# Kernel optimization log

Measured on AMD Instinct MI355X. Metric: run time of the kernel, lower is better.

## Reference

```python
import jax, jax.numpy as jnp
import numpy as np

N = 500000
C = 128
G = 4096


def setup_inputs() -> dict:
    key = jax.random.key(0)
    ks = jax.random.split(key, 6)
    x = jax.random.normal(ks[0], (N, C), dtype=jnp.float32)
    proj_w = jax.random.normal(ks[1], (C, C), dtype=jnp.float32) * (1.0 / np.sqrt(C))
    proj_b = jax.random.normal(ks[2], (C,), dtype=jnp.float32) * 0.01
    score_w = jax.random.normal(ks[3], (1, C), dtype=jnp.float32) * (1.0 / np.sqrt(C))
    score_b = jax.random.normal(ks[4], (1,), dtype=jnp.float32) * 0.01
    batch = jnp.sort(jax.random.randint(ks[5], (N,), 0, G, dtype=jnp.int32))
    return {"x": x, "proj_w": proj_w, "proj_b": proj_b,
            "score_w": score_w, "score_b": score_b,
            "batch": batch, "num_graphs": G}


def reference(x, proj_w, proj_b, score_w, score_b, batch, num_graphs):
    # h = tanh(Linear(x)); s = Linear(h) -> [N]
    h = jnp.tanh(x @ proj_w.T + proj_b)
    s = (h @ score_w.T + score_b)[:, 0]  # [N]
    # segment softmax over nodes of each graph
    m = jax.ops.segment_max(s, batch, num_segments=num_graphs)  # [G]
    m = jnp.where(jnp.isfinite(m), m, 0.0)  # guard empty segments
    e = jnp.exp(s - m[batch])
    denom = jax.ops.segment_sum(e, batch, num_segments=num_graphs)  # [G]
    w = e / jnp.maximum(denom[batch], 1e-30)  # [N]
    # weighted scatter-sum of raw features
    pooled = jax.ops.segment_sum(x * w[:, None], batch, num_segments=num_graphs)  # [G, C]
    return pooled
```

## Files before the change

### kernel.cpp

```cpp
#include <hip/hip_runtime.h>
#include <hip/hip_bf16.h>
#include <float.h>
#include <math.h>

#define CDIM 128

typedef __attribute__((ext_vector_type(8))) short short8v;
typedef __attribute__((ext_vector_type(4))) short short4v;
typedef __attribute__((ext_vector_type(4))) float f32x4;

__device__ __forceinline__ short bf16b(float f) {
    __hip_bfloat16 h = __float2bfloat16(f);
    return __builtin_bit_cast(short, h);
}

__device__ __forceinline__ float tanh_fast(float y) {
    float e = __expf(2.0f * y);
    return 1.0f - 2.0f / (e + 1.0f);
}

__device__ __forceinline__ int lower_bound_i(const int* __restrict__ b, int n, int v) {
    int lo = 0, hi = n;
    while (lo < hi) { int mid = (lo + hi) >> 1; if (b[mid] < v) lo = mid + 1; else hi = mid; }
    return lo;
}

__global__ void seg_bounds_kernel(const int* __restrict__ batch, int N, int G,
                                  int* __restrict__ seg) {
    int g = blockIdx.x * blockDim.x + threadIdx.x;
    if (g < G) seg[g] = lower_bound_i(batch, N, g);
    if (g == 0) seg[G] = N;
}

__global__ void wconv_kernel(const float* __restrict__ proj_w, short* __restrict__ wfrag) {
    int tid = blockIdx.x * 256 + threadIdx.x;
    int f = tid >> 6, l = tid & 63;
    int c  = ((f >> 2) << 4) | (l & 15);
    int k0 = ((f & 3) << 5) | ((l >> 4) << 3);
    short8v v;
    #pragma unroll
    for (int j = 0; j < 8; ++j) v[j] = bf16b(proj_w[c * CDIM + k0 + j]);
    ((short8v*)wfrag)[tid] = v;
}

__launch_bounds__(256, 4)
__global__ void pool_kernel(const float* __restrict__ x,
                            const short* __restrict__ wfrag,
                            const float* __restrict__ proj_b,
                            const float* __restrict__ score_w,
                            const float* __restrict__ score_b,
                            const int* __restrict__ seg,
                            float* __restrict__ out,
                            int N) {
    __shared__ __align__(16) short XsB[64 * 128];
    __shared__ float ps[64 * 4];

    const int g = blockIdx.x;
    const int t = threadIdx.x;
    const int lane = t & 63;
    const int w = t >> 6;
    const int start = seg[g];
    const int cnt = seg[g + 1] - start;
    float4* og4 = (float4*)(out + (size_t)g * CDIM);

    if (cnt <= 0) {
        if (t < 32) og4[t] = make_float4(0.f, 0.f, 0.f, 0.f);
        return;
    }

    short8v wf[2][4];
    {
        const short8v* wfg = (const short8v*)wfrag;
        #pragma unroll
        for (int j = 0; j < 2; ++j)
            #pragma unroll
            for (int ks = 0; ks < 4; ++ks)
                wf[j][ks] = wfg[((((w << 1) | j) << 2 | ks) << 6) | lane];
    }
    const int al = lane & 15, ah = lane >> 4;
    float swl[2], pbl[2];
    #pragma unroll
    for (int j = 0; j < 2; ++j) {
        swl[j] = score_w[(((w << 1) | j) << 4) + al];
        pbl[j] = proj_b[(((w << 1) | j) << 4) + al];
    }
    const float sb = score_b[0];

    const float4* __restrict__ x4 = (const float4*)x;
    const int g8 = t >> 5;
    const int c4 = t & 31;

    float m_run = -FLT_MAX, l_run = 0.0f;
    float4 pa = make_float4(0.f, 0.f, 0.f, 0.f);

    for (int cb = 0; cb < cnt; cb += 64) {
        const int rem = cnt - cb;

        float4 xr[8];
        #pragma unroll
        for (int i = 0; i < 8; ++i) {
            int row = g8 + (i << 3);
            size_t gr = (size_t)min(start + cb + row, N - 1);
            xr[i] = x4[gr * 32 + c4];
        }
        #pragma unroll
        for (int i = 0; i < 8; ++i) {
            int row = g8 + (i << 3);
            short4v b;
            b[0] = bf16b(xr[i].x); b[1] = bf16b(xr[i].y);
            b[2] = bf16b(xr[i].z); b[3] = bf16b(xr[i].w);
            *(short4v*)&XsB[(row << 7) | ((c4 << 2) ^ ((row & 7) << 3))] = b;
        }
        __syncthreads();

        #pragma unroll
        for (int rt = 0; rt < 4; ++rt) {
            const int arow = (rt << 4) | al;
            const int rsw = (arow & 7) << 3;
            f32x4 a0 = (f32x4){0.f, 0.f, 0.f, 0.f};
            f32x4 a1 = (f32x4){0.f, 0.f, 0.f, 0.f};
            #pragma unroll
            for (int ks = 0; ks < 4; ++ks) {
                short8v af = *(const short8v*)&XsB[(arow << 7) | (((ks << 5) | (ah << 3)) ^ rsw)];
                a0 = __builtin_amdgcn_mfma_f32_16x16x32_bf16(af, wf[0][ks], a0, 0, 0, 0);
                a1 = __builtin_amdgcn_mfma_f32_16x16x32_bf16(af, wf[1][ks], a1, 0, 0, 0);
            }
            #pragma unroll
            for (int r = 0; r < 4; ++r) {
                float s = swl[0] * tanh_fast(a0[r] + pbl[0])
                        + swl[1] * tanh_fast(a1[r] + pbl[1]);
                s += __shfl_xor(s, 1); s += __shfl_xor(s, 2);
                s += __shfl_xor(s, 4); s += __shfl_xor(s, 8);
                if (al == 0) ps[(((rt << 4) | (ah << 2) | r) << 2) | w] = s;
            }
        }
        __syncthreads();

        float4 pp = *(const float4*)&ps[lane << 2];
        float sv = (lane < rem) ? (pp.x + pp.y + pp.z + pp.w + sb) : -FLT_MAX;
        float mx = sv;
        #pragma unroll
        for (int m = 1; m < 64; m <<= 1) mx = fmaxf(mx, __shfl_xor(mx, m));
        const float m_new = fmaxf(m_run, mx);
        float ev = (lane < rem) ? __expf(sv - m_new) : 0.f;
        float ssum = ev;
        #pragma unroll
        for (int m = 1; m < 64; m <<= 1) ssum += __shfl_xor(ssum, m);
        const float sc = __expf(m_run - m_new);
        m_run = m_new;
        l_run = l_run * sc + ssum;
        pa.x *= sc; pa.y *= sc; pa.z *= sc; pa.w *= sc;

        #pragma unroll
        for (int i = 0; i < 8; ++i) {
            float em = __shfl(ev, g8 + (i << 3));
            pa.x += em * xr[i].x; pa.y += em * xr[i].y;
            pa.z += em * xr[i].z; pa.w += em * xr[i].w;
        }
    }

    float* red = (float*)XsB;
    *(float4*)&red[(g8 << 7) + (c4 << 2)] = pa;
    __syncthreads();
    if (t < 32) {
        float4 v = make_float4(0.f, 0.f, 0.f, 0.f);
        #pragma unroll
        for (int j = 0; j < 8; ++j) {
            float4 r = *(const float4*)&red[(j << 7) + (t << 2)];
            v.x += r.x; v.y += r.y; v.z += r.z; v.w += r.w;
        }
        const float inv = 1.0f / fmaxf(l_run, 1e-30f);
        v.x *= inv; v.y *= inv; v.z *= inv; v.w *= inv;
        og4[t] = v;
    }
}

extern "C" void kernel_launch(void* const* d_in, const int* in_sizes, int n_in,
                              void* d_out, int out_size, void* d_ws, size_t ws_size,
                              hipStream_t stream) {
    const float* x       = (const float*)d_in[0];
    const float* proj_w  = (const float*)d_in[1];
    const float* proj_b  = (const float*)d_in[2];
    const float* score_w = (const float*)d_in[3];
    const float* score_b = (const float*)d_in[4];
    const int*   batch   = (const int*)d_in[5];

    const int N = in_sizes[0] / CDIM;
    const int G = out_size / CDIM;

    int*   seg   = (int*)d_ws;
    short* wfrag = (short*)((char*)d_ws + (((size_t)(G + 1) * 4 + 255) & ~(size_t)255));

    seg_bounds_kernel<<<(G + 255) / 256, 256, 0, stream>>>(batch, N, G, seg);
    wconv_kernel<<<8, 256, 0, stream>>>(proj_w, wfrag);
    pool_kernel<<<G, 256, 0, stream>>>(x, wfrag, proj_b, score_w, score_b,
                                       seg, (float*)d_out, N);
}
```

Before: 100.5 us.

## Double-buffer x chunks in LDS via async global_load_lds prefetch

After: 104.5 us. +4.0%, slower.

```diff
diff --git a/kernel.cpp b/kernel.cpp
--- a/kernel.cpp
+++ b/kernel.cpp
@@ -6,7 +6,6 @@
 #define CDIM 128
 
 typedef __attribute__((ext_vector_type(8))) short short8v;
-typedef __attribute__((ext_vector_type(4))) short short4v;
 typedef __attribute__((ext_vector_type(4))) float f32x4;
 
 __device__ __forceinline__ short bf16b(float f) {
@@ -43,6 +42,22 @@
     ((short8v*)wfrag)[tid] = v;
 }
 
+__device__ __forceinline__ void dma_rows(const float* __restrict__ x, float* dst_base,
+                                         int w, int lane, int row0, int rem) {
+    #pragma unroll
+    for (int j = 0; j < 4; ++j) {
+        const int T = (w << 2) | j;
+        const int row = (T << 1) | (lane >> 5);
+        const int f4 = lane & 31;
+        const size_t gr = (size_t)(row0 + min(row, rem - 1));
+        const float* src = x + (gr << 7) + ((f4 ^ (row & 7)) << 2);
+        __builtin_amdgcn_global_load_lds(
+            (__attribute__((address_space(1))) const void*)src,
+            (__attribute__((address_space(3))) void*)(dst_base + (T << 8)),
+            16, 0, 0);
+    }
+}
+
 __launch_bounds__(256, 4)
 __global__ void pool_kernel(const float* __restrict__ x,
                             const short* __restrict__ wfrag,
@@ -52,8 +67,8 @@
                             const int* __restrict__ seg,
                             float* __restrict__ out,
                             int N) {
-    __shared__ __align__(16) short XsB[64 * 128];
-    __shared__ float ps[64 * 4];
+    __shared__ __align__(16) float Xf[2][32 * 128];
+    __shared__ float ps[32 * 4];
 
     const int g = blockIdx.x;
     const int t = threadIdx.x;
@@ -68,6 +83,8 @@
         return;
     }
 
+    dma_rows(x, Xf[0], w, lane, start, cnt);
+
     short8v wf[2][4];
     {
         const short8v* wfg = (const short8v*)wfrag;
@@ -77,7 +94,7 @@
             for (int ks = 0; ks < 4; ++ks)
                 wf[j][ks] = wfg[((((w << 1) | j) << 2 | ks) << 6) | lane];
     }
-    const int al = lane & 15, ah = lane >> 4;
+    const int al = lane & 15, kq = lane >> 4;
     float swl[2], pbl[2];
     #pragma unroll
     for (int j = 0; j < 2; ++j) {
@@ -86,42 +103,40 @@
     }
     const float sb = score_b[0];
 
-    const float4* __restrict__ x4 = (const float4*)x;
-    const int g8 = t >> 5;
+    const int rp = t >> 5;
     const int c4 = t & 31;
 
     float m_run = -FLT_MAX, l_run = 0.0f;
     float4 pa = make_float4(0.f, 0.f, 0.f, 0.f);
 
-    for (int cb = 0; cb < cnt; cb += 64) {
-        const int rem = cnt - cb;
-
-        float4 xr[8];
-        #pragma unroll
-        for (int i = 0; i < 8; ++i) {
-            int row = g8 + (i << 3);
-            size_t gr = (size_t)min(start + cb + row, N - 1);
-            xr[i] = x4[gr * 32 + c4];
-        }
-        #pragma unroll
-        for (int i = 0; i < 8; ++i) {
-            int row = g8 + (i << 3);
-            short4v b;
-            b[0] = bf16b(xr[i].x); b[1] = bf16b(xr[i].y);
-            b[2] = bf16b(xr[i].z); b[3] = bf16b(xr[i].w);
-            *(short4v*)&XsB[(row << 7) | ((c4 << 2) ^ ((row & 7) << 3))] = b;
-        }
-        __syncthreads();
-
-        #pragma unroll
-        for (int rt = 0; rt < 4; ++rt) {
+    const int nchunks = (cnt + 31) >> 5;
+    __syncthreads();
+
+    int bsel = 0;
+    for (int c = 0; c < nchunks; ++c) {
+        const float* A = Xf[bsel];
+        const float4* Av = (const float4*)A;
+        const int rem_c = min(32, cnt - (c << 5));
+
+        if (c + 1 < nchunks)
+            dma_rows(x, Xf[bsel ^ 1], w, lane, start + ((c + 1) << 5), cnt - ((c + 1) << 5));
+
+        #pragma unroll
+        for (int rt = 0; rt < 2; ++rt) {
             const int arow = (rt << 4) | al;
-            const int rsw = (arow & 7) << 3;
+            const int swz = arow & 7;
             f32x4 a0 = (f32x4){0.f, 0.f, 0.f, 0.f};
             f32x4 a1 = (f32x4){0.f, 0.f, 0.f, 0.f};
             #pragma unroll
             for (int ks = 0; ks < 4; ++ks) {
-                short8v af = *(const short8v*)&XsB[(arow << 7) | (((ks << 5) | (ah << 3)) ^ rsw)];
+                const int fb = (ks << 3) | (kq << 1);
+                float4 q0 = Av[(arow << 5) | (fb ^ swz)];
+                float4 q1 = Av[(arow << 5) | ((fb + 1) ^ swz)];
+                short8v af;
+                af[0] = bf16b(q0.x); af[1] = bf16b(q0.y);
+                af[2] = bf16b(q0.z); af[3] = bf16b(q0.w);
+                af[4] = bf16b(q1.x); af[5] = bf16b(q1.y);
+                af[6] = bf16b(q1.z); af[7] = bf16b(q1.w);
                 a0 = __builtin_amdgcn_mfma_f32_16x16x32_bf16(af, wf[0][ks], a0, 0, 0, 0);
                 a1 = __builtin_amdgcn_mfma_f32_16x16x32_bf16(af, wf[1][ks], a1, 0, 0, 0);
             }
@@ -131,18 +146,21 @@
                         + swl[1] * tanh_fast(a1[r] + pbl[1]);
                 s += __shfl_xor(s, 1); s += __shfl_xor(s, 2);
                 s += __shfl_xor(s, 4); s += __shfl_xor(s, 8);
-                if (al == 0) ps[(((rt << 4) | (ah << 2) | r) << 2) | w] = s;
+                if (al == 0) ps[(((rt << 4) | (kq << 2) | r) << 2) | w] = s;
             }
         }
         __syncthreads();
 
-        float4 pp = *(const float4*)&ps[lane << 2];
-        float sv = (lane < rem) ? (pp.x + pp.y + pp.z + pp.w + sb) : -FLT_MAX;
+        float sv = -FLT_MAX;
+        if (lane < rem_c) {
+            float4 pp = *(const float4*)&ps[lane << 2];
+            sv = pp.x + pp.y + pp.z + pp.w + sb;
+        }
         float mx = sv;
         #pragma unroll
         for (int m = 1; m < 64; m <<= 1) mx = fmaxf(mx, __shfl_xor(mx, m));
         const float m_new = fmaxf(m_run, mx);
-        float ev = (lane < rem) ? __expf(sv - m_new) : 0.f;
+        float ev = (lane < rem_c) ? __expf(sv - m_new) : 0.f;
         float ssum = ev;
         #pragma unroll
         for (int m = 1; m < 64; m <<= 1) ssum += __shfl_xor(ssum, m);
@@ -152,21 +170,24 @@
         pa.x *= sc; pa.y *= sc; pa.z *= sc; pa.w *= sc;
 
         #pragma unroll
-        for (int i = 0; i < 8; ++i) {
-            float em = __shfl(ev, g8 + (i << 3));
-            pa.x += em * xr[i].x; pa.y += em * xr[i].y;
-            pa.z += em * xr[i].z; pa.w += em * xr[i].w;
-        }
-    }
-
-    float* red = (float*)XsB;
-    *(float4*)&red[(g8 << 7) + (c4 << 2)] = pa;
+        for (int i = 0; i < 4; ++i) {
+            const int row = rp | (i << 3);
+            const float em = __shfl(ev, row);
+            float4 xv = Av[(row << 5) | (c4 ^ (row & 7))];
+            pa.x += em * xv.x; pa.y += em * xv.y;
+            pa.z += em * xv.z; pa.w += em * xv.w;
+        }
+        __syncthreads();
+        bsel ^= 1;
+    }
+
+    *(float4*)&Xf[0][t << 2] = pa;
     __syncthreads();
     if (t < 32) {
         float4 v = make_float4(0.f, 0.f, 0.f, 0.f);
         #pragma unroll
         for (int j = 0; j < 8; ++j) {
-            float4 r = *(const float4*)&red[(j << 7) + (t << 2)];
+            float4 r = *(const float4*)&Xf[0][((j << 5) | t) << 2];
             v.x += r.x; v.y += r.y; v.z += r.z; v.w += r.w;
         }
         const float inv = 1.0f / fmaxf(l_run, 1e-30f);
```
